# Performance work log

Hardware: AMD Instinct MI355X
Metric: run time of the kernel (lower is better)

## Reference

```python
import jax, jax.numpy as jnp
import numpy as np

B, T, C = 32, 4096, 256


def setup_inputs() -> dict:
    key = jax.random.key(0)
    ks = jax.random.split(key, 10)
    s = lambda *sh: 0.05
    return {
        "gru_output": jax.random.normal(ks[0], (B, T, C), jnp.float32),
        "intensity_curves": jax.random.uniform(ks[1], (B, T), jnp.float32),
        "W1": jax.random.normal(ks[2], (C, 128), jnp.float32) * 0.05,
        "b1": jnp.zeros((128,), jnp.float32),
        "W2": jax.random.normal(ks[3], (128, 64), jnp.float32) * 0.05,
        "b2": jnp.zeros((64,), jnp.float32),
        "W3": jax.random.normal(ks[4], (64, 4), jnp.float32) * 0.05,
        "b3": jnp.zeros((4,), jnp.float32),
        "conv_w": jax.random.normal(ks[5], (1, C, 3), jnp.float32) * 0.05,  # OIH
        "conv_b": jnp.zeros((1,), jnp.float32),
    }


def reference(gru_output, intensity_curves, W1, b1, W2, b2, W3, b3, conv_w, conv_b):
    Bb, Tt, Cc = gru_output.shape
    # per-timestep phase classifier MLP + softmax -> (B,T,4)
    h = jax.nn.relu(gru_output @ W1 + b1)
    h = jax.nn.relu(h @ W2 + b2)
    phase_probs = jax.nn.softmax(h @ W3 + b3, axis=-1)
    # transition scores: Conv1d(C->1,k=3,pad=1) + sigmoid -> (B,T)
    x = jnp.transpose(gru_output, (0, 2, 1))  # (B,C,T)
    ts = jax.lax.conv_general_dilated(x, conv_w, (1,), 'SAME',
                                      dimension_numbers=('NCH', 'OIH', 'NCH'))
    transition_scores = jax.nn.sigmoid(ts[:, 0, :] + conv_b[0])  # (B,T)
    # run-length segments: new segment when dominant phase changes or transition>0.7
    dom = jnp.argmax(phase_probs, axis=-1)  # (B,T) int
    change = (dom[:, 1:] != dom[:, :-1]) | (transition_scores[:, 1:] > 0.7)
    change = jnp.concatenate([jnp.zeros((Bb, 1), bool), change], axis=1)
    seg = jnp.cumsum(change.astype(jnp.int32), axis=1)  # (B,T) segment id per step
    gseg = (seg + jnp.arange(Bb, dtype=jnp.int32)[:, None] * Tt).reshape(-1)
    nseg = Bb * Tt
    cnt = jax.ops.segment_sum(jnp.ones((nseg,), jnp.float32)[: gseg.shape[0]] * 0 + 1.0,
                              gseg, num_segments=nseg)
    sum_int = jax.ops.segment_sum(intensity_curves.reshape(-1), gseg, num_segments=nseg)
    conf_t = jnp.take_along_axis(phase_probs, dom[..., None], axis=2)[..., 0]  # (B,T)
    sum_conf = jax.ops.segment_sum(conf_t.reshape(-1), gseg, num_segments=nseg)
    denom = jnp.maximum(cnt, 1.0)
    mean_int = (sum_int / denom)[gseg].reshape(Bb, Tt)   # segment-mean intensity per step
    mean_conf = (sum_conf / denom)[gseg].reshape(Bb, Tt)  # segment-mean confidence per step
    return phase_probs, transition_scores, seg, mean_int, mean_conf
```

## Files before the change

### kernel.cpp

```cpp
#include <hip/hip_runtime.h>

#define B_ 32
#define T_ 4096
#define C_ 256
#define R_ (B_*T_)
#define H1_ 128
#define H2_ 64

#define TB 64

#define PROBS_OFF 0
#define TS_OFF  (R_*4)
#define SEG_OFF (TS_OFF + R_)
#define MI_OFF  (SEG_OFF + R_)
#define MC_OFF  (MI_OFF + R_)

#define XS_OFF  0
#define XS_P    268
#define H1S_OFF 0
#define H1S_P   132
#define W2S_OFF 8448
#define W1S_OFF 17152
#define SMEMF   19200

__device__ __forceinline__ void fma4(float4& a, float s, const float4& b) {
  a.x = fmaf(s, b.x, a.x); a.y = fmaf(s, b.y, a.y);
  a.z = fmaf(s, b.z, a.z); a.w = fmaf(s, b.w, a.w);
}

__global__ __launch_bounds__(256, 2) void mlp_conv_kernel(
    const float* __restrict__ X, const float* __restrict__ W1, const float* __restrict__ b1,
    const float* __restrict__ W2, const float* __restrict__ b2,
    const float* __restrict__ W3, const float* __restrict__ b3,
    const float* __restrict__ CW, const float* __restrict__ CB,
    float* __restrict__ out)
{
  __shared__ float sm[SMEMF];
  const int tid  = threadIdx.x;
  const int l    = tid & 63;
  const int w    = tid >> 6;
  const int row0 = blockIdx.x * TB;

  float4 st0 = ((const float4*)W1)[tid];
  float4 st1 = ((const float4*)W1)[tid + 256];

  #pragma unroll
  for (int i2 = 0; i2 < 16; ++i2) {
    int g = tid + 256 * i2;
    int r = g >> 6, m = g & 63;
    float4 v = *(const float4*)&X[(size_t)(row0 + r) * C_ + m * 4];
    *(float4*)&sm[XS_OFF + r * XS_P + m * 4] = v;
  }
  __syncthreads();

  #pragma unroll
  for (int half = 0; half < 2; ++half) {
    const int rowi = half * 32 + w * 8 + (l & 7);
    const int p = l >> 3;
    const int grow = row0 + rowi;
    const int tb = grow & (T_ - 1);
    float s = 0.f;
    #pragma unroll
    for (int cc = 0; cc < 8; ++cc) {
      const int c = p * 32 + cc * 4;
      float4 x0 = *(const float4*)&sm[XS_OFF + rowi * XS_P + c];
      float4 xm, xp;
      if (tb == 0)             xm = make_float4(0.f, 0.f, 0.f, 0.f);
      else if (rowi >= 1)      xm = *(const float4*)&sm[XS_OFF + (rowi - 1) * XS_P + c];
      else                     xm = *(const float4*)&X[(size_t)(grow - 1) * C_ + c];
      if (tb == T_ - 1)        xp = make_float4(0.f, 0.f, 0.f, 0.f);
      else if (rowi + 1 < TB)  xp = *(const float4*)&sm[XS_OFF + (rowi + 1) * XS_P + c];
      else                     xp = *(const float4*)&X[(size_t)(grow + 1) * C_ + c];
      float4 wa = *(const float4*)&CW[c * 3 + 0];
      float4 wb = *(const float4*)&CW[c * 3 + 4];
      float4 wc = *(const float4*)&CW[c * 3 + 8];
      s += xm.x * wa.x + x0.x * wa.y + xp.x * wa.z;
      s += xm.y * wa.w + x0.y * wb.x + xp.y * wb.y;
      s += xm.z * wb.z + x0.z * wb.w + xp.z * wc.x;
      s += xm.w * wc.y + x0.w * wc.z + xp.w * wc.w;
    }
    s += __shfl_xor(s, 8);
    s += __shfl_xor(s, 16);
    s += __shfl_xor(s, 32);
    if (p == 0) out[TS_OFF + grow] = 1.f / (1.f + expf(-(s + CB[0])));
  }

  const int rt = tid >> 5, ct = tid & 31;
  const int rb = rt * 8;
  float4 acc[8];
  #pragma unroll
  for (int r = 0; r < 8; ++r) acc[r] = make_float4(0.f, 0.f, 0.f, 0.f);

  for (int kc = 0; kc < 16; ++kc) {
    *(float4*)&sm[W1S_OFF + tid * 4]         = st0;
    *(float4*)&sm[W1S_OFF + (tid + 256) * 4] = st1;
    __syncthreads();
    if (kc + 1 < 16) {
      const float* wp = W1 + (size_t)(kc + 1) * 2048;
      st0 = ((const float4*)wp)[tid];
      st1 = ((const float4*)wp)[tid + 256];
    } else {
      st0 = ((const float4*)W2)[tid];
      st1 = ((const float4*)W2)[tid + 256];
    }
    #pragma unroll
    for (int k4 = 0; k4 < 4; ++k4) {
      const int kb = kc * 16 + k4 * 4;
      float4 a0 = *(const float4*)&sm[XS_OFF + (rb + 0) * XS_P + kb];
      float4 a1 = *(const float4*)&sm[XS_OFF + (rb + 1) * XS_P + kb];
      float4 a2 = *(const float4*)&sm[XS_OFF + (rb + 2) * XS_P + kb];
      float4 a3 = *(const float4*)&sm[XS_OFF + (rb + 3) * XS_P + kb];
      float4 a4 = *(const float4*)&sm[XS_OFF + (rb + 4) * XS_P + kb];
      float4 a5 = *(const float4*)&sm[XS_OFF + (rb + 5) * XS_P + kb];
      float4 a6 = *(const float4*)&sm[XS_OFF + (rb + 6) * XS_P + kb];
      float4 a7 = *(const float4*)&sm[XS_OFF + (rb + 7) * XS_P + kb];
      float4 q0 = *(const float4*)&sm[W1S_OFF + (k4 * 4 + 0) * H1_ + ct * 4];
      float4 q1 = *(const float4*)&sm[W1S_OFF + (k4 * 4 + 1) * H1_ + ct * 4];
      float4 q2 = *(const float4*)&sm[W1S_OFF + (k4 * 4 + 2) * H1_ + ct * 4];
      float4 q3 = *(const float4*)&sm[W1S_OFF + (k4 * 4 + 3) * H1_ + ct * 4];
      fma4(acc[0], a0.x, q0); fma4(acc[0], a0.y, q1); fma4(acc[0], a0.z, q2); fma4(acc[0], a0.w, q3);
      fma4(acc[1], a1.x, q0); fma4(acc[1], a1.y, q1); fma4(acc[1], a1.z, q2); fma4(acc[1], a1.w, q3);
      fma4(acc[2], a2.x, q0); fma4(acc[2], a2.y, q1); fma4(acc[2], a2.z, q2); fma4(acc[2], a2.w, q3);
      fma4(acc[3], a3.x, q0); fma4(acc[3], a3.y, q1); fma4(acc[3], a3.z, q2); fma4(acc[3], a3.w, q3);
      fma4(acc[4], a4.x, q0); fma4(acc[4], a4.y, q1); fma4(acc[4], a4.z, q2); fma4(acc[4], a4.w, q3);
      fma4(acc[5], a5.x, q0); fma4(acc[5], a5.y, q1); fma4(acc[5], a5.z, q2); fma4(acc[5], a5.w, q3);
      fma4(acc[6], a6.x, q0); fma4(acc[6], a6.y, q1); fma4(acc[6], a6.z, q2); fma4(acc[6], a6.w, q3);
      fma4(acc[7], a7.x, q0); fma4(acc[7], a7.y, q1); fma4(acc[7], a7.z, q2); fma4(acc[7], a7.w, q3);
    }
    __syncthreads();
  }

  const int rt2 = tid >> 4, ct2 = tid & 15;
  float4 w2r[6];
  #pragma unroll
  for (int i = 0; i < 6; ++i) w2r[i] = ((const float4*)W2)[tid + 512 + 256 * i];
  float4 w30 = ((const float4*)W3)[ct2 * 4 + 0];
  float4 w31 = ((const float4*)W3)[ct2 * 4 + 1];
  float4 w32 = ((const float4*)W3)[ct2 * 4 + 2];
  float4 w33 = ((const float4*)W3)[ct2 * 4 + 3];
  float4 b3v = *(const float4*)&b3[0];

  {
    float4 bb = ((const float4*)b1)[ct];
    #pragma unroll
    for (int r = 0; r < 8; ++r) {
      float4 h = acc[r];
      h.x = fmaxf(h.x + bb.x, 0.f); h.y = fmaxf(h.y + bb.y, 0.f);
      h.z = fmaxf(h.z + bb.z, 0.f); h.w = fmaxf(h.w + bb.w, 0.f);
      *(float4*)&sm[H1S_OFF + (rb + r) * H1S_P + ct * 4] = h;
    }
  }
  *(float4*)&sm[W2S_OFF + tid * 4]         = st0;
  *(float4*)&sm[W2S_OFF + (tid + 256) * 4] = st1;
  #pragma unroll
  for (int i = 0; i < 6; ++i)
    *(float4*)&sm[W2S_OFF + (tid + 512 + 256 * i) * 4] = w2r[i];
  __syncthreads();

  float4 acc2[4];
  #pragma unroll
  for (int j = 0; j < 4; ++j) acc2[j] = make_float4(0.f, 0.f, 0.f, 0.f);
  #pragma unroll 4
  for (int k4 = 0; k4 < 32; ++k4) {
    float4 a0 = *(const float4*)&sm[H1S_OFF + (rt2 * 4 + 0) * H1S_P + k4 * 4];
    float4 a1 = *(const float4*)&sm[H1S_OFF + (rt2 * 4 + 1) * H1S_P + k4 * 4];
    float4 a2 = *(const float4*)&sm[H1S_OFF + (rt2 * 4 + 2) * H1S_P + k4 * 4];
    float4 a3 = *(const float4*)&sm[H1S_OFF + (rt2 * 4 + 3) * H1S_P + k4 * 4];
    float4 q0 = *(const float4*)&sm[W2S_OFF + (k4 * 4 + 0) * H2_ + ct2 * 4];
    float4 q1 = *(const float4*)&sm[W2S_OFF + (k4 * 4 + 1) * H2_ + ct2 * 4];
    float4 q2 = *(const float4*)&sm[W2S_OFF + (k4 * 4 + 2) * H2_ + ct2 * 4];
    float4 q3 = *(const float4*)&sm[W2S_OFF + (k4 * 4 + 3) * H2_ + ct2 * 4];
    fma4(acc2[0], a0.x, q0); fma4(acc2[0], a0.y, q1); fma4(acc2[0], a0.z, q2); fma4(acc2[0], a0.w, q3);
    fma4(acc2[1], a1.x, q0); fma4(acc2[1], a1.y, q1); fma4(acc2[1], a1.z, q2); fma4(acc2[1], a1.w, q3);
    fma4(acc2[2], a2.x, q0); fma4(acc2[2], a2.y, q1); fma4(acc2[2], a2.z, q2); fma4(acc2[2], a2.w, q3);
    fma4(acc2[3], a3.x, q0); fma4(acc2[3], a3.y, q1); fma4(acc2[3], a3.z, q2); fma4(acc2[3], a3.w, q3);
  }

  float4 L[4];
  {
    float4 bb = ((const float4*)b2)[ct2];
    #pragma unroll
    for (int r = 0; r < 4; ++r) {
      float4 h = acc2[r];
      h.x = fmaxf(h.x + bb.x, 0.f); h.y = fmaxf(h.y + bb.y, 0.f);
      h.z = fmaxf(h.z + bb.z, 0.f); h.w = fmaxf(h.w + bb.w, 0.f);
      float4 t = make_float4(0.f, 0.f, 0.f, 0.f);
      fma4(t, h.x, w30); fma4(t, h.y, w31); fma4(t, h.z, w32); fma4(t, h.w, w33);
      L[r] = t;
    }
  }
  #pragma unroll
  for (int d = 1; d < 16; d <<= 1) {
    #pragma unroll
    for (int r = 0; r < 4; ++r) {
      L[r].x += __shfl_xor(L[r].x, d);
      L[r].y += __shfl_xor(L[r].y, d);
      L[r].z += __shfl_xor(L[r].z, d);
      L[r].w += __shfl_xor(L[r].w, d);
    }
  }

  if (ct2 < 4) {
    float4 Lv = L[ct2];
    const int grow = row0 + rt2 * 4 + ct2;
    Lv.x += b3v.x; Lv.y += b3v.y; Lv.z += b3v.z; Lv.w += b3v.w;
    float mx = fmaxf(fmaxf(Lv.x, Lv.y), fmaxf(Lv.z, Lv.w));
    float e0 = expf(Lv.x - mx), e1 = expf(Lv.y - mx), e2 = expf(Lv.z - mx), e3 = expf(Lv.w - mx);
    float inv = 1.f / ((e0 + e1) + (e2 + e3));
    float p0 = e0 * inv, p1 = e1 * inv, p2 = e2 * inv, p3 = e3 * inv;
    *(float4*)&out[PROBS_OFF + (size_t)grow * 4] = make_float4(p0, p1, p2, p3);
    int dom = 0; float pm = p0;
    if (p1 > pm) { pm = p1; dom = 1; }
    if (p2 > pm) { pm = p2; dom = 2; }
    if (p3 > pm) { pm = p3; dom = 3; }
    out[MI_OFF + grow] = (float)dom;
    out[MC_OFF + grow] = pm;
  }
}

__global__ __launch_bounds__(1024, 1) void seg_kernel(
    const float* __restrict__ inten, float* __restrict__ out)
{
  __shared__ float scnt[T_], ssi[T_], ssc[T_];
  __shared__ int wtot[16], wexcl[16];
  const int tid = threadIdx.x;
  const int lane = tid & 63, wid = tid >> 6;
  const size_t base = (size_t)blockIdx.x * T_;
  const float* tsS = out + TS_OFF;
  float* segO = out + SEG_OFF;
  float* miO  = out + MI_OFF;
  float* mcO  = out + MC_OFF;
  const int t4 = tid * 4;

  float4 dv = *(const float4*)&miO[base + t4];
  float4 tv = *(const float4*)&tsS[base + t4];
  float4 iv = *(const float4*)&inten[base + t4];
  float4 cv = *(const float4*)&mcO[base + t4];
  float pd = (tid == 0) ? 0.f : miO[base + t4 - 1];

  for (int i = tid; i < T_; i += 1024) { scnt[i] = 0.f; ssi[i] = 0.f; ssc[i] = 0.f; }

  int c0 = (t4 == 0) ? 0 : (((dv.x != pd)   || (tv.x > 0.7f)) ? 1 : 0);
  int c1 = ((dv.y != dv.x) || (tv.y > 0.7f)) ? 1 : 0;
  int c2 = ((dv.z != dv.y) || (tv.z > 0.7f)) ? 1 : 0;
  int c3 = ((dv.w != dv.z) || (tv.w > 0.7f)) ? 1 : 0;
  int l0 = c0, l1 = c0 + c1, l2 = l1 + c2, l3 = l2 + c3;
  const int tsum = l3;

  int v = tsum;
  #pragma unroll
  for (int d = 1; d < 64; d <<= 1) {
    int o = __shfl_up(v, (unsigned)d);
    if (lane >= d) v += o;
  }
  if (lane == 63) wtot[wid] = v;
  __syncthreads();
  if (tid < 16) {
    int x = wtot[tid];
    int xx = x;
    #pragma unroll
    for (int d = 1; d < 16; d <<= 1) {
      int o = __shfl_up(xx, (unsigned)d);
      if (tid >= d) xx += o;
    }
    wexcl[tid] = xx - x;
  }
  __syncthreads();
  const int texcl = wexcl[wid] + (v - tsum);
  const int s0 = texcl + l0, s1 = texcl + l1, s2 = texcl + l2, s3 = texcl + l3;

  {
    int cur = s0; float aI = iv.x, aC = cv.x, aN = 1.f;
    if (s1 == cur) { aI += iv.y; aC += cv.y; aN += 1.f; }
    else { atomicAdd(&ssi[cur], aI); atomicAdd(&ssc[cur], aC); atomicAdd(&scnt[cur], aN);
           cur = s1; aI = iv.y; aC = cv.y; aN = 1.f; }
    if (s2 == cur) { aI += iv.z; aC += cv.z; aN += 1.f; }
    else { atomicAdd(&ssi[cur], aI); atomicAdd(&ssc[cur], aC); atomicAdd(&scnt[cur], aN);
           cur = s2; aI = iv.z; aC = cv.z; aN = 1.f; }
    if (s3 == cur) { aI += iv.w; aC += cv.w; aN += 1.f; }
    else { atomicAdd(&ssi[cur], aI); atomicAdd(&ssc[cur], aC); atomicAdd(&scnt[cur], aN);
           cur = s3; aI = iv.w; aC = cv.w; aN = 1.f; }
    atomicAdd(&ssi[cur], aI); atomicAdd(&ssc[cur], aC); atomicAdd(&scnt[cur], aN);
  }
  __syncthreads();

  float n0 = scnt[s0], n1 = scnt[s1], n2 = scnt[s2], n3 = scnt[s3];
  float4 m4, q4, g4;
  m4.x = ssi[s0] / n0; m4.y = ssi[s1] / n1; m4.z = ssi[s2] / n2; m4.w = ssi[s3] / n3;
  q4.x = ssc[s0] / n0; q4.y = ssc[s1] / n1; q4.z = ssc[s2] / n2; q4.w = ssc[s3] / n3;
  g4.x = (float)s0; g4.y = (float)s1; g4.z = (float)s2; g4.w = (float)s3;
  *(float4*)&segO[base + t4] = g4;
  *(float4*)&miO[base + t4]  = m4;
  *(float4*)&mcO[base + t4]  = q4;
}

extern "C" void kernel_launch(void* const* d_in, const int* in_sizes, int n_in,
                              void* d_out, int out_size, void* d_ws, size_t ws_size,
                              hipStream_t stream) {
  (void)in_sizes; (void)n_in; (void)out_size; (void)d_ws; (void)ws_size;
  const float* X   = (const float*)d_in[0];
  const float* INT = (const float*)d_in[1];
  const float* W1  = (const float*)d_in[2];
  const float* B1  = (const float*)d_in[3];
  const float* W2  = (const float*)d_in[4];
  const float* B2  = (const float*)d_in[5];
  const float* W3  = (const float*)d_in[6];
  const float* B3  = (const float*)d_in[7];
  const float* CW  = (const float*)d_in[8];
  const float* CB  = (const float*)d_in[9];
  float* out = (float*)d_out;

  hipLaunchKernelGGL(mlp_conv_kernel, dim3(R_ / TB), dim3(256), 0, stream,
                     X, W1, B1, W2, B2, W3, B3, CW, CB, out);
  hipLaunchKernelGGL(seg_kernel, dim3(B_), dim3(1024), 0, stream, INT, out);
}
```

Before: 179.5 us.

## Stream W1 directly from global into registers instead of staging in LDS

The first GEMM no longer copies W1 chunks into shared memory with a barrier per chunk. Each thread loads its own W1 column slice straight from global (L1/L2-cached) into registers, prefetching the next k-step while computing the current one. This removes 32 barriers and the LDS traffic for W1, and the X tile row pitch shrinks to reduce LDS size. In exchange it relies on cache hits for redundant W1 global loads across threads, and the new 260 pitch may change LDS bank-conflict behaviour.

```diff
diff --git a/kernel.cpp b/kernel.cpp
--- a/kernel.cpp
+++ b/kernel.cpp
@@ -16,12 +16,11 @@
 #define MC_OFF  (MI_OFF + R_)
 
 #define XS_OFF  0
-#define XS_P    268
+#define XS_P    260
 #define H1S_OFF 0
 #define H1S_P   132
 #define W2S_OFF 8448
-#define W1S_OFF 17152
-#define SMEMF   19200
+#define SMEMF   16640
 
 __device__ __forceinline__ void fma4(float4& a, float s, const float4& b) {
   a.x = fmaf(s, b.x, a.x); a.y = fmaf(s, b.y, a.y);
@@ -40,9 +39,6 @@
   const int l    = tid & 63;
   const int w    = tid >> 6;
   const int row0 = blockIdx.x * TB;
-
-  float4 st0 = ((const float4*)W1)[tid];
-  float4 st1 = ((const float4*)W1)[tid + 256];
 
   #pragma unroll
   for (int i2 = 0; i2 < 16; ++i2) {
@@ -87,25 +83,23 @@
 
   const int rt = tid >> 5, ct = tid & 31;
   const int rb = rt * 8;
+  const float* wb1 = W1 + ct * 4;
   float4 acc[8];
   #pragma unroll
   for (int r = 0; r < 8; ++r) acc[r] = make_float4(0.f, 0.f, 0.f, 0.f);
-
-  for (int kc = 0; kc < 16; ++kc) {
-    *(float4*)&sm[W1S_OFF + tid * 4]         = st0;
-    *(float4*)&sm[W1S_OFF + (tid + 256) * 4] = st1;
-    __syncthreads();
-    if (kc + 1 < 16) {
-      const float* wp = W1 + (size_t)(kc + 1) * 2048;
-      st0 = ((const float4*)wp)[tid];
-      st1 = ((const float4*)wp)[tid + 256];
-    } else {
-      st0 = ((const float4*)W2)[tid];
-      st1 = ((const float4*)W2)[tid + 256];
-    }
-    #pragma unroll
-    for (int k4 = 0; k4 < 4; ++k4) {
-      const int kb = kc * 16 + k4 * 4;
+  {
+    float4 Bc0 = *(const float4*)&wb1[(size_t)0 * H1_];
+    float4 Bc1 = *(const float4*)&wb1[(size_t)1 * H1_];
+    float4 Bc2 = *(const float4*)&wb1[(size_t)2 * H1_];
+    float4 Bc3 = *(const float4*)&wb1[(size_t)3 * H1_];
+    #pragma unroll 2
+    for (int k4 = 0; k4 < 64; ++k4) {
+      const int kn = (k4 < 63) ? (k4 + 1) * 4 : 252;
+      float4 Bn0 = *(const float4*)&wb1[(size_t)(kn + 0) * H1_];
+      float4 Bn1 = *(const float4*)&wb1[(size_t)(kn + 1) * H1_];
+      float4 Bn2 = *(const float4*)&wb1[(size_t)(kn + 2) * H1_];
+      float4 Bn3 = *(const float4*)&wb1[(size_t)(kn + 3) * H1_];
+      const int kb = k4 * 4;
       float4 a0 = *(const float4*)&sm[XS_OFF + (rb + 0) * XS_P + kb];
       float4 a1 = *(const float4*)&sm[XS_OFF + (rb + 1) * XS_P + kb];
       float4 a2 = *(const float4*)&sm[XS_OFF + (rb + 2) * XS_P + kb];
@@ -114,31 +108,29 @@
       float4 a5 = *(const float4*)&sm[XS_OFF + (rb + 5) * XS_P + kb];
       float4 a6 = *(const float4*)&sm[XS_OFF + (rb + 6) * XS_P + kb];
       float4 a7 = *(const float4*)&sm[XS_OFF + (rb + 7) * XS_P + kb];
-      float4 q0 = *(const float4*)&sm[W1S_OFF + (k4 * 4 + 0) * H1_ + ct * 4];
-      float4 q1 = *(const float4*)&sm[W1S_OFF + (k4 * 4 + 1) * H1_ + ct * 4];
-      float4 q2 = *(const float4*)&sm[W1S_OFF + (k4 * 4 + 2) * H1_ + ct * 4];
-      float4 q3 = *(const float4*)&sm[W1S_OFF + (k4 * 4 + 3) * H1_ + ct * 4];
-      fma4(acc[0], a0.x, q0); fma4(acc[0], a0.y, q1); fma4(acc[0], a0.z, q2); fma4(acc[0], a0.w, q3);
-      fma4(acc[1], a1.x, q0); fma4(acc[1], a1.y, q1); fma4(acc[1], a1.z, q2); fma4(acc[1], a1.w, q3);
-      fma4(acc[2], a2.x, q0); fma4(acc[2], a2.y, q1); fma4(acc[2], a2.z, q2); fma4(acc[2], a2.w, q3);
-      fma4(acc[3], a3.x, q0); fma4(acc[3], a3.y, q1); fma4(acc[3], a3.z, q2); fma4(acc[3], a3.w, q3);
-      fma4(acc[4], a4.x, q0); fma4(acc[4], a4.y, q1); fma4(acc[4], a4.z, q2); fma4(acc[4], a4.w, q3);
-      fma4(acc[5], a5.x, q0); fma4(acc[5], a5.y, q1); fma4(acc[5], a5.z, q2); fma4(acc[5], a5.w, q3);
-      fma4(acc[6], a6.x, q0); fma4(acc[6], a6.y, q1); fma4(acc[6], a6.z, q2); fma4(acc[6], a6.w, q3);
-      fma4(acc[7], a7.x, q0); fma4(acc[7], a7.y, q1); fma4(acc[7], a7.z, q2); fma4(acc[7], a7.w, q3);
-    }
-    __syncthreads();
+      fma4(acc[0], a0.x, Bc0); fma4(acc[0], a0.y, Bc1); fma4(acc[0], a0.z, Bc2); fma4(acc[0], a0.w, Bc3);
+      fma4(acc[1], a1.x, Bc0); fma4(acc[1], a1.y, Bc1); fma4(acc[1], a1.z, Bc2); fma4(acc[1], a1.w, Bc3);
+      fma4(acc[2], a2.x, Bc0); fma4(acc[2], a2.y, Bc1); fma4(acc[2], a2.z, Bc2); fma4(acc[2], a2.w, Bc3);
+      fma4(acc[3], a3.x, Bc0); fma4(acc[3], a3.y, Bc1); fma4(acc[3], a3.z, Bc2); fma4(acc[3], a3.w, Bc3);
+      fma4(acc[4], a4.x, Bc0); fma4(acc[4], a4.y, Bc1); fma4(acc[4], a4.z, Bc2); fma4(acc[4], a4.w, Bc3);
+      fma4(acc[5], a5.x, Bc0); fma4(acc[5], a5.y, Bc1); fma4(acc[5], a5.z, Bc2); fma4(acc[5], a5.w, Bc3);
+      fma4(acc[6], a6.x, Bc0); fma4(acc[6], a6.y, Bc1); fma4(acc[6], a6.z, Bc2); fma4(acc[6], a6.w, Bc3);
+      fma4(acc[7], a7.x, Bc0); fma4(acc[7], a7.y, Bc1); fma4(acc[7], a7.z, Bc2); fma4(acc[7], a7.w, Bc3);
+      Bc0 = Bn0; Bc1 = Bn1; Bc2 = Bn2; Bc3 = Bn3;
+    }
   }
 
   const int rt2 = tid >> 4, ct2 = tid & 15;
-  float4 w2r[6];
-  #pragma unroll
-  for (int i = 0; i < 6; ++i) w2r[i] = ((const float4*)W2)[tid + 512 + 256 * i];
+  float4 w2q[8];
+  #pragma unroll
+  for (int i = 0; i < 8; ++i) w2q[i] = ((const float4*)W2)[tid + 256 * i];
   float4 w30 = ((const float4*)W3)[ct2 * 4 + 0];
   float4 w31 = ((const float4*)W3)[ct2 * 4 + 1];
   float4 w32 = ((const float4*)W3)[ct2 * 4 + 2];
   float4 w33 = ((const float4*)W3)[ct2 * 4 + 3];
+  float4 b2v = ((const float4*)b2)[ct2];
   float4 b3v = *(const float4*)&b3[0];
+  __syncthreads();
 
   {
     float4 bb = ((const float4*)b1)[ct];
@@ -150,11 +142,9 @@
       *(float4*)&sm[H1S_OFF + (rb + r) * H1S_P + ct * 4] = h;
     }
   }
-  *(float4*)&sm[W2S_OFF + tid * 4]         = st0;
-  *(float4*)&sm[W2S_OFF + (tid + 256) * 4] = st1;
-  #pragma unroll
-  for (int i = 0; i < 6; ++i)
-    *(float4*)&sm[W2S_OFF + (tid + 512 + 256 * i) * 4] = w2r[i];
+  #pragma unroll
+  for (int i = 0; i < 8; ++i)
+    *(float4*)&sm[W2S_OFF + (tid + 256 * i) * 4] = w2q[i];
   __syncthreads();
 
   float4 acc2[4];
@@ -178,12 +168,11 @@
 
   float4 L[4];
   {
-    float4 bb = ((const float4*)b2)[ct2];
     #pragma unroll
     for (int r = 0; r < 4; ++r) {
       float4 h = acc2[r];
-      h.x = fmaxf(h.x + bb.x, 0.f); h.y = fmaxf(h.y + bb.y, 0.f);
-      h.z = fmaxf(h.z + bb.z, 0.f); h.w = fmaxf(h.w + bb.w, 0.f);
+      h.x = fmaxf(h.x + b2v.x, 0.f); h.y = fmaxf(h.y + b2v.y, 0.f);
+      h.z = fmaxf(h.z + b2v.z, 0.f); h.w = fmaxf(h.w + b2v.w, 0.f);
       float4 t = make_float4(0.f, 0.f, 0.f, 0.f);
       fma4(t, h.x, w30); fma4(t, h.y, w31); fma4(t, h.z, w32); fma4(t, h.w, w33);
       L[r] = t;
```

After: 186.1 us. 1.04x slower.
